# Optimization experiments

Measured on AMD Instinct MI355X. Metric: run time of the kernel, lower is better.

The kernel has to match this reference:

```python
import jax, jax.numpy as jnp
import numpy as np

LOW, HIGH, SIZE = 0.0, 1.0, 32


def setup_inputs() -> dict:
    key = jax.random.key(0)
    x = jax.random.uniform(key, (1_000_000,), dtype=jnp.float32)
    return {"x": x}


def reference(x):
    # thresholds: interior points of linspace(low, high, size+2)
    th = jnp.linspace(LOW, HIGH, SIZE + 2, dtype=x.dtype)[1:-1]  # [SIZE]
    x = jnp.reshape(x, (-1,))
    n = x.shape[0]
    x_prev = x[:-1, None]  # [N-1, 1]
    x_next = x[1:, None]   # [N-1, 1]
    up = (x_prev <= th) & (x_next > th)    # [N-1, SIZE]
    down = (x_prev > th) & (x_next <= th)  # [N-1, SIZE]
    # interleave up/down per threshold -> columns [2j, 2j+1]
    inter = jnp.stack([up, down], axis=-1).reshape(n - 1, 2 * SIZE).astype(jnp.float32)
    # original allocates N rows; last row (index N-1) is never written -> zeros
    spike_times = jnp.concatenate([inter, jnp.zeros((1, 2 * SIZE), dtype=jnp.float32)], axis=0)
    return spike_times
```

## Files before the change

### kernel.cpp

```cpp
#include <hip/hip_runtime.h>
#include <hip/hip_bf16.h>


typedef float f32x4 __attribute__((ext_vector_type(4)));

__global__ __launch_bounds__(256) void ThresholdEncode_kernel(
    const float* __restrict__ x, f32x4* __restrict__ out, int n) {
    const int t = blockIdx.x * 256 + threadIdx.x;
    const int ngroups = (n + 7) >> 3;
    if (t >= ngroups * 16) return;
    const int c  = t & 15;
    const int g  = t >> 4;
    const int j0 = g << 3;

    const float t0 = (float)((double)(2 * c + 1) * (1.0 / 33.0));
    const float t1 = (float)((double)(2 * c + 2) * (1.0 / 33.0));

    float xv[9];
    if (j0 + 8 <= n) {
        const f32x4 a = *(const f32x4*)(x + j0);
        const f32x4 b = *(const f32x4*)(x + j0 + 4);
        xv[0]=a.x; xv[1]=a.y; xv[2]=a.z; xv[3]=a.w;
        xv[4]=b.x; xv[5]=b.y; xv[6]=b.z; xv[7]=b.w;
        xv[8] = (j0 + 8 < n) ? x[j0 + 8] : 0.0f;
    } else {
        #pragma unroll
        for (int k = 0; k < 9; ++k) xv[k] = (j0 + k < n) ? x[j0 + k] : 0.0f;
    }

    #pragma unroll
    for (int k = 0; k < 8; ++k) {
        const int j = j0 + k;
        if (j >= n) break;
        f32x4 v = (f32x4)(0.f, 0.f, 0.f, 0.f);
        if (j < n - 1) {
            const float xp = xv[k];
            const float xn = xv[k + 1];
            v.x = (xp <= t0 && xn >  t0) ? 1.0f : 0.0f;
            v.y = (xp >  t0 && xn <= t0) ? 1.0f : 0.0f;
            v.z = (xp <= t1 && xn >  t1) ? 1.0f : 0.0f;
            v.w = (xp >  t1 && xn <= t1) ? 1.0f : 0.0f;
        }
        out[j * 16 + c] = v;
    }
}

extern "C" void kernel_launch(void* const* d_in, const int* in_sizes, int n_in,
                              void* d_out, int out_size, void* d_ws, size_t ws_size,
                              hipStream_t stream) {
    const float* x = (const float*)d_in[0];
    f32x4* out = (f32x4*)d_out;
    const int n = in_sizes[0];
    const int ngroups = (n + 7) >> 3;
    const int threads = ngroups * 16;
    const int block = 256;
    const int grid = (threads + block - 1) / block;
    ThresholdEncode_kernel<<<grid, block, 0, stream>>>(x, out, n);
}
```

Baseline: 244.6 us.

## Convert to grid-stride loop with fixed grid and prefetch of next input group

Replaces the one-thread-per-group launch with a fixed grid of 2048 blocks in which each thread walks groups with a grid stride. It loads the next group's inputs before computing and storing the current one, so load latency overlaps the stores. This targets block launch overhead and exposed load latency. The output is write-bound (256 MB), so the gain may be small, and the fixed grid could underfill or overfill the device.

```diff
diff --git a/kernel.cpp b/kernel.cpp
--- a/kernel.cpp
+++ b/kernel.cpp
@@ -6,42 +6,60 @@
 
 __global__ __launch_bounds__(256) void ThresholdEncode_kernel(
     const float* __restrict__ x, f32x4* __restrict__ out, int n) {
+    const int nthreads = gridDim.x * 256;
     const int t = blockIdx.x * 256 + threadIdx.x;
     const int ngroups = (n + 7) >> 3;
-    if (t >= ngroups * 16) return;
-    const int c  = t & 15;
-    const int g  = t >> 4;
-    const int j0 = g << 3;
+    const int gstride = nthreads >> 4;
+    const int c = t & 15;
 
     const float t0 = (float)((double)(2 * c + 1) * (1.0 / 33.0));
     const float t1 = (float)((double)(2 * c + 2) * (1.0 / 33.0));
 
-    float xv[9];
-    if (j0 + 8 <= n) {
-        const f32x4 a = *(const f32x4*)(x + j0);
-        const f32x4 b = *(const f32x4*)(x + j0 + 4);
-        xv[0]=a.x; xv[1]=a.y; xv[2]=a.z; xv[3]=a.w;
-        xv[4]=b.x; xv[5]=b.y; xv[6]=b.z; xv[7]=b.w;
-        xv[8] = (j0 + 8 < n) ? x[j0 + 8] : 0.0f;
-    } else {
+    auto loadg = [&](int gg, f32x4& A, f32x4& B, float& E) {
+        const int j0 = gg << 3;
+        if (j0 + 8 <= n) {
+            A = *(const f32x4*)(x + j0);
+            B = *(const f32x4*)(x + j0 + 4);
+            E = (j0 + 8 < n) ? x[j0 + 8] : 0.0f;
+        } else {
+            float tmp[9];
+            #pragma unroll
+            for (int k = 0; k < 9; ++k) tmp[k] = (j0 + k < n) ? x[j0 + k] : 0.0f;
+            A = (f32x4)(tmp[0], tmp[1], tmp[2], tmp[3]);
+            B = (f32x4)(tmp[4], tmp[5], tmp[6], tmp[7]);
+            E = tmp[8];
+        }
+    };
+
+    int g = t >> 4;
+    if (g >= ngroups) return;
+
+    f32x4 A, B; float E;
+    loadg(g, A, B, E);
+
+    for (; g < ngroups; g += gstride) {
+        const int gn = g + gstride;
+        f32x4 A2, B2; float E2 = 0.0f;
+        if (gn < ngroups) loadg(gn, A2, B2, E2);
+
+        const int j0 = g << 3;
+        float xv[9] = {A.x, A.y, A.z, A.w, B.x, B.y, B.z, B.w, E};
+
+        f32x4* o = out + (size_t)j0 * 16 + c;
         #pragma unroll
-        for (int k = 0; k < 9; ++k) xv[k] = (j0 + k < n) ? x[j0 + k] : 0.0f;
-    }
-
-    #pragma unroll
-    for (int k = 0; k < 8; ++k) {
-        const int j = j0 + k;
-        if (j >= n) break;
-        f32x4 v = (f32x4)(0.f, 0.f, 0.f, 0.f);
-        if (j < n - 1) {
-            const float xp = xv[k];
-            const float xn = xv[k + 1];
-            v.x = (xp <= t0 && xn >  t0) ? 1.0f : 0.0f;
-            v.y = (xp >  t0 && xn <= t0) ? 1.0f : 0.0f;
-            v.z = (xp <= t1 && xn >  t1) ? 1.0f : 0.0f;
-            v.w = (xp >  t1 && xn <= t1) ? 1.0f : 0.0f;
+        for (int k = 0; k < 8; ++k) {
+            f32x4 v = (f32x4)(0.f, 0.f, 0.f, 0.f);
+            if (j0 + k < n - 1) {
+                const float xp = xv[k];
+                const float xn = xv[k + 1];
+                v.x = (xp <= t0 && xn >  t0) ? 1.0f : 0.0f;
+                v.y = (xp >  t0 && xn <= t0) ? 1.0f : 0.0f;
+                v.z = (xp <= t1 && xn >  t1) ? 1.0f : 0.0f;
+                v.w = (xp >  t1 && xn <= t1) ? 1.0f : 0.0f;
+            }
+            if (j0 + k < n) o[k * 16] = v;
         }
-        out[j * 16 + c] = v;
+        A = A2; B = B2; E = E2;
     }
 }
 
@@ -51,9 +69,7 @@
     const float* x = (const float*)d_in[0];
     f32x4* out = (f32x4*)d_out;
     const int n = in_sizes[0];
-    const int ngroups = (n + 7) >> 3;
-    const int threads = ngroups * 16;
     const int block = 256;
-    const int grid = (threads + block - 1) / block;
+    const int grid = 2048;
     ThresholdEncode_kernel<<<grid, block, 0, stream>>>(x, out, n);
 }
```

Result: no change. 245.2 us (+0.2%).
